# Performance work log

Measured on AMD Instinct MI355X. Metric: run time of the kernel, lower is better.

## Reference

```python
import jax, jax.numpy as jnp
import numpy as np

N_SPECIES = 2
N_RBF = 16
HIDDEN = 64
CUTOFF = 2.5


def setup_inputs() -> dict:
    key = jax.random.key(0)
    ks = jax.random.split(key, 10)
    B, N = 8, 1024
    positions = jax.random.uniform(ks[0], (B, N, 3), dtype=jnp.float32) * 10.0
    types = jax.random.randint(ks[1], (B, N), 0, N_SPECIES)
    in_dim = N_SPECIES + N_SPECIES * N_RBF  # 34
    def lin(k, fan_in, fan_out):
        bound = 1.0 / np.sqrt(fan_in)
        kw, kb = jax.random.split(k)
        W = jax.random.uniform(kw, (fan_in, fan_out), minval=-bound, maxval=bound, dtype=jnp.float32)
        b = jax.random.uniform(kb, (fan_out,), minval=-bound, maxval=bound, dtype=jnp.float32)
        return W, b
    W1, b1 = lin(ks[2], in_dim, 64)
    W2, b2 = lin(ks[3], 64, 64)
    W3, b3 = lin(ks[4], 64, HIDDEN)
    return {"positions": positions, "types": types,
            "W1": W1, "b1": b1, "W2": W2, "b2": b2, "W3": W3, "b3": b3}


def _forward(positions, types, W1, b1, W2, b2, W3, b3):
    B, N, _ = positions.shape
    # pairwise distances with safe sqrt (zero grad on diagonal, matching torch norm subgradient)
    disp = positions[:, :, None, :] - positions[:, None, :, :]          # [B,N,N,3]
    sq = jnp.sum(disp * disp, axis=-1)                                   # [B,N,N]
    nz = sq > 0.0
    d = jnp.sqrt(jnp.where(nz, sq, 1.0)) * nz
    # RBF expansion
    centers = jnp.linspace(0.0, CUTOFF, N_RBF)
    widths = jnp.full((N_RBF,), CUTOFF / max(N_RBF - 1, 1))
    diff = d[..., None] - centers                                        # [B,N,N,R]
    rbf = jnp.exp(-(diff ** 2) / (widths ** 2 + 1e-12))
    # smooth polynomial cutoff
    x = d / CUTOFF
    cut = jnp.where(d < CUTOFF, 1.0 - 6.0 * x ** 5 + 15.0 * x ** 4 - 10.0 * x ** 3, 0.0)
    rbf = rbf * cut[..., None]
    eye = jnp.eye(N, dtype=bool)[None, :, :, None]
    rbf = jnp.where(eye, 0.0, rbf)
    # species-weighted neighbor aggregation
    onehot = jax.nn.one_hot(types, N_SPECIES, dtype=positions.dtype)      # [B,N,S]
    env = jnp.einsum('bijr,bjs->birs', rbf, onehot).reshape(B, N, -1)     # [B,N,R*S]
    feats = jnp.concatenate([onehot, env], axis=-1)                       # [B,N,S+S*R]
    h = jax.nn.silu(feats @ W1 + b1)
    h = jax.nn.silu(h @ W2 + b2)
    return h @ W3 + b3                                                    # [B,N,HIDDEN]


def reference(positions, types, W1, b1, W2, b2, W3, b3):
    return _forward(positions, types, W1, b1, W2, b2, W3, b3)
```

## Files before the change

kernel.cpp:

```cpp
#include <hip/hip_runtime.h>
#include <hip/hip_bf16.h>

#define NTHREADS 256
#define N_ATOMS  1024
#define HIDDEN   64
#define SEGCAP   272

__global__ __launch_bounds__(NTHREADS) void LocalFeatureEncoder_40063454937486_kernel(
    const float* __restrict__ pos,
    const int*   __restrict__ types,
    const float* __restrict__ W1,
    const float* __restrict__ b1,
    const float* __restrict__ W2,
    const float* __restrict__ b2,
    const float* __restrict__ W3,
    const float* __restrict__ b3,
    float*       __restrict__ out)
{
    const int a    = blockIdx.x;
    const int bidx = a >> 10;
    const int i    = a & (N_ATOMS - 1);
    const int tid  = threadIdx.x;
    const int lane = tid & 63;
    const int wav  = tid >> 6;

    __shared__ float2 qdm[4 * SEGCAP];
    __shared__ float2 part2[4 * 16];
    __shared__ int    nseg[4];
    __shared__ float  feats[64];
    __shared__ float  h1s[64];
    __shared__ float  h2s[64];

    const float* pf   = pos + (size_t)bidx * (N_ATOMS * 3);
    const int*   typb = types + (size_t)bidx * N_ATOMS;

    const float4 p0 = *(const float4*)(pf + tid * 12);
    const float4 p1 = *(const float4*)(pf + tid * 12 + 4);
    const float4 p2 = *(const float4*)(pf + tid * 12 + 8);
    const int4   tv = *(const int4*)(typb + tid * 4);

    const float xi = pf[i * 3 + 0];
    const float yi = pf[i * 3 + 1];
    const float zi = pf[i * 3 + 2];

    {
        const float px[4] = {p0.x, p0.w, p1.z, p2.y};
        const float py[4] = {p0.y, p1.x, p1.w, p2.z};
        const float pz[4] = {p0.z, p1.y, p2.x, p2.w};
        const int   tj[4] = {tv.x, tv.y, tv.z, tv.w};
        float2* seg = &qdm[wav * SEGCAP];
        int base = 0;

#pragma unroll
        for (int q = 0; q < 4; ++q) {
            const int j = tid * 4 + q;
            const float dx = xi - px[q], dy = yi - py[q], dz = zi - pz[q];
            const float sq = dx * dx + dy * dy + dz * dz;
            const bool pred = (j != i) && (sq < 6.25f);

            const unsigned long long mask = __ballot(pred);
            if (pred) {
                const float d  = sqrtf(sq);
                const float x  = d * 0.4f;
                const float x3 = x * x * x;
                const float cutv = 1.0f + x3 * (-10.0f + x * (15.0f - 6.0f * x));
                const int idx = base + (int)__popcll(mask & ((1ull << lane) - 1ull));
                seg[idx] = make_float2(d, (tj[q] == 0) ? cutv : -cutv);
            }
            base += (int)__popcll(mask);
        }
        const int npad = (base + 15) & ~15;
        if (lane < npad - base) seg[base + lane] = make_float2(0.0f, 0.0f);
        if (lane == 0) nseg[wav] = npad;
    }
    __syncthreads();

    {
        const int   p = tid >> 4;
        const int   r = tid & 15;
        const float c = (float)r * (2.5f / 15.0f);

        float acc0 = 0.0f, acc1 = 0.0f;
#pragma unroll
        for (int w = 0; w < 4; ++w) {
            const int n = nseg[w];
            const float2* s = &qdm[w * SEGCAP];
            for (int e = p; e < n; e += 16) {
                const float2 dm  = s[e];
                const float diff = dm.x - c;
                const float ex   = __expf(diff * diff * -36.0f);
                acc0 += ex * fmaxf(dm.y, 0.0f);
                acc1 += ex * fmaxf(-dm.y, 0.0f);
            }
        }
        acc0 += __shfl_xor(acc0, 16, 64);
        acc0 += __shfl_xor(acc0, 32, 64);
        acc1 += __shfl_xor(acc1, 16, 64);
        acc1 += __shfl_xor(acc1, 32, 64);
        if (lane < 16) part2[wav * 16 + lane] = make_float2(acc0, acc1);
    }
    __syncthreads();

    if (tid < 16) {
        const float2 a0 = part2[tid];
        const float2 a1 = part2[16 + tid];
        const float2 a2 = part2[32 + tid];
        const float2 a3 = part2[48 + tid];
        feats[2 + 2 * tid + 0] = a0.x + a1.x + a2.x + a3.x;
        feats[2 + 2 * tid + 1] = a0.y + a1.y + a2.y + a3.y;
    }
    if (tid == 16) {
        const int ti = typb[i];
        feats[0] = (ti == 0) ? 1.0f : 0.0f;
        feats[1] = (ti == 1) ? 1.0f : 0.0f;
    }
    __syncthreads();

    if (tid < HIDDEN) {
        float h = b1[tid];
#pragma unroll
        for (int k = 0; k < 34; k++) h += feats[k] * W1[k * HIDDEN + tid];
        h = h / (1.0f + __expf(-h));
        h1s[tid] = h;
    }
    __syncthreads();
    if (tid < HIDDEN) {
        float h = b2[tid];
#pragma unroll
        for (int k = 0; k < HIDDEN; k++) h += h1s[k] * W2[k * HIDDEN + tid];
        h = h / (1.0f + __expf(-h));
        h2s[tid] = h;
    }
    __syncthreads();
    if (tid < HIDDEN) {
        float o = b3[tid];
#pragma unroll
        for (int k = 0; k < HIDDEN; k++) o += h2s[k] * W3[k * HIDDEN + tid];
        out[(size_t)a * HIDDEN + tid] = o;
    }
}

extern "C" void kernel_launch(void* const* d_in, const int* in_sizes, int n_in,
                              void* d_out, int out_size, void* d_ws, size_t ws_size,
                              hipStream_t stream) {
    const float* pos   = (const float*)d_in[0];
    const int*   types = (const int*)d_in[1];
    const float* W1    = (const float*)d_in[2];
    const float* b1    = (const float*)d_in[3];
    const float* W2    = (const float*)d_in[4];
    const float* b2    = (const float*)d_in[5];
    const float* W3    = (const float*)d_in[6];
    const float* b3    = (const float*)d_in[7];
    float*       out   = (float*)d_out;

    const int BN = in_sizes[1];

    LocalFeatureEncoder_40063454937486_kernel<<<BN, NTHREADS, 0, stream>>>(
        pos, types, W1, b1, W2, b2, W3, b3, out);
}
```

Measured before the change: 89.34 us.

## Map one atom per wavefront, stage positions in LDS, use shuffles for MLP

Changes the work split from one atom per 256-thread block to one atom per 64-lane wavefront, with four atoms per block. The block stages all positions and types of its batch in shared memory. Each wave compacts its own neighbour list by scanning all 1024 atoms, evaluates the RBF and cutoff terms from packed signed distances, and runs the three MLP layers with wave shuffles instead of shared-memory barriers. This cuts redundant position loads and MLP-phase idle threads, but each wave now does the full neighbour scan serially and MLP weights are loaded per wave.

```diff
diff --git a/kernel.cpp b/kernel.cpp
--- a/kernel.cpp
+++ b/kernel.cpp
@@ -4,7 +4,7 @@
 #define NTHREADS 256
 #define N_ATOMS  1024
 #define HIDDEN   64
-#define SEGCAP   272
+#define SEGCAP   512
 
 __global__ __launch_bounds__(NTHREADS) void LocalFeatureEncoder_40063454937486_kernel(
     const float* __restrict__ pos,
@@ -17,127 +17,120 @@
     const float* __restrict__ b3,
     float*       __restrict__ out)
 {
-    const int a    = blockIdx.x;
-    const int bidx = a >> 10;
-    const int i    = a & (N_ATOMS - 1);
     const int tid  = threadIdx.x;
     const int lane = tid & 63;
     const int wav  = tid >> 6;
+    const int a    = blockIdx.x * 4 + wav;
+    const int bidx = blockIdx.x >> 8;
+    const int i    = a & (N_ATOMS - 1);
 
-    __shared__ float2 qdm[4 * SEGCAP];
-    __shared__ float2 part2[4 * 16];
-    __shared__ int    nseg[4];
-    __shared__ float  feats[64];
-    __shared__ float  h1s[64];
-    __shared__ float  h2s[64];
+    __shared__ float sx[N_ATOMS];
+    __shared__ float sy[N_ATOMS];
+    __shared__ float sz[N_ATOMS];
+    __shared__ float st[N_ATOMS];
+    __shared__ float qv[4 * SEGCAP];
 
     const float* pf   = pos + (size_t)bidx * (N_ATOMS * 3);
     const int*   typb = types + (size_t)bidx * N_ATOMS;
 
-    const float4 p0 = *(const float4*)(pf + tid * 12);
-    const float4 p1 = *(const float4*)(pf + tid * 12 + 4);
-    const float4 p2 = *(const float4*)(pf + tid * 12 + 8);
-    const int4   tv = *(const int4*)(typb + tid * 4);
+    {
+        const float4 p0 = *(const float4*)(pf + tid * 12);
+        const float4 p1 = *(const float4*)(pf + tid * 12 + 4);
+        const float4 p2 = *(const float4*)(pf + tid * 12 + 8);
+        const int4   tv = *(const int4*)(typb + tid * 4);
 
-    const float xi = pf[i * 3 + 0];
-    const float yi = pf[i * 3 + 1];
-    const float zi = pf[i * 3 + 2];
-
-    {
         const float px[4] = {p0.x, p0.w, p1.z, p2.y};
         const float py[4] = {p0.y, p1.x, p1.w, p2.z};
         const float pz[4] = {p0.z, p1.y, p2.x, p2.w};
         const int   tj[4] = {tv.x, tv.y, tv.z, tv.w};
-        float2* seg = &qdm[wav * SEGCAP];
-        int base = 0;
-
 #pragma unroll
         for (int q = 0; q < 4; ++q) {
             const int j = tid * 4 + q;
-            const float dx = xi - px[q], dy = yi - py[q], dz = zi - pz[q];
-            const float sq = dx * dx + dy * dy + dz * dz;
-            const bool pred = (j != i) && (sq < 6.25f);
-
-            const unsigned long long mask = __ballot(pred);
-            if (pred) {
-                const float d  = sqrtf(sq);
-                const float x  = d * 0.4f;
-                const float x3 = x * x * x;
-                const float cutv = 1.0f + x3 * (-10.0f + x * (15.0f - 6.0f * x));
-                const int idx = base + (int)__popcll(mask & ((1ull << lane) - 1ull));
-                seg[idx] = make_float2(d, (tj[q] == 0) ? cutv : -cutv);
-            }
-            base += (int)__popcll(mask);
+            sx[j] = px[q];
+            sy[j] = py[q];
+            sz[j] = pz[q];
+            st[j] = (tj[q] == 0) ? 1.0f : -1.0f;
         }
-        const int npad = (base + 15) & ~15;
-        if (lane < npad - base) seg[base + lane] = make_float2(0.0f, 0.0f);
-        if (lane == 0) nseg[wav] = npad;
     }
     __syncthreads();
 
-    {
-        const int   p = tid >> 4;
-        const int   r = tid & 15;
-        const float c = (float)r * (2.5f / 15.0f);
+    const float xi = sx[i];
+    const float yi = sy[i];
+    const float zi = sz[i];
 
-        float acc0 = 0.0f, acc1 = 0.0f;
+    float* seg = &qv[wav * SEGCAP];
+    int base = 0;
 #pragma unroll
-        for (int w = 0; w < 4; ++w) {
-            const int n = nseg[w];
-            const float2* s = &qdm[w * SEGCAP];
-            for (int e = p; e < n; e += 16) {
-                const float2 dm  = s[e];
-                const float diff = dm.x - c;
-                const float ex   = __expf(diff * diff * -36.0f);
-                acc0 += ex * fmaxf(dm.y, 0.0f);
-                acc1 += ex * fmaxf(-dm.y, 0.0f);
-            }
+    for (int s = 0; s < N_ATOMS / 64; ++s) {
+        const int j = lane + s * 64;
+        const float dx = xi - sx[j];
+        const float dy = yi - sy[j];
+        const float dz = zi - sz[j];
+        const float sq = dx * dx + dy * dy + dz * dz;
+        const bool pred = (j != i) && (sq < 6.25f);
+
+        const unsigned long long mask = __ballot(pred);
+        if (pred) {
+            const float d = sqrtf(sq);
+            const int idx = base + (int)__popcll(mask & ((1ull << lane) - 1ull));
+            seg[idx] = (st[j] > 0.0f) ? d : -d;
         }
-        acc0 += __shfl_xor(acc0, 16, 64);
-        acc0 += __shfl_xor(acc0, 32, 64);
-        acc1 += __shfl_xor(acc1, 16, 64);
-        acc1 += __shfl_xor(acc1, 32, 64);
-        if (lane < 16) part2[wav * 16 + lane] = make_float2(acc0, acc1);
+        base += (int)__popcll(mask);
     }
+    const int npad = (base + 3) & ~3;
+    if (lane < npad - base) seg[base + lane] = 100.0f;
     __syncthreads();
 
-    if (tid < 16) {
-        const float2 a0 = part2[tid];
-        const float2 a1 = part2[16 + tid];
-        const float2 a2 = part2[32 + tid];
-        const float2 a3 = part2[48 + tid];
-        feats[2 + 2 * tid + 0] = a0.x + a1.x + a2.x + a3.x;
-        feats[2 + 2 * tid + 1] = a0.y + a1.y + a2.y + a3.y;
+    float acc0 = 0.0f, acc1 = 0.0f;
+    {
+        const int   p = lane >> 4;
+        const int   r = lane & 15;
+        const float c = (float)r * (2.5f / 15.0f);
+        const int   slot = p;
+        for (int e = slot; e < npad; e += 4) {
+            const float v   = seg[e];
+            const float d   = fabsf(v);
+            const float sgn = __builtin_copysignf(1.0f, v);
+            const float x   = d * 0.4f;
+            const float x3  = x * x * x;
+            const float cutv = 1.0f + x3 * (-10.0f + x * (15.0f - 6.0f * x));
+            const float diff = d - c;
+            const float ex   = __expf(diff * diff * -36.0f);
+            const float m0 = (sgn > 0.0f) ? cutv : 0.0f;
+            const float m1 = (sgn > 0.0f) ? 0.0f : cutv;
+            acc0 += ex * m0;
+            acc1 += ex * m1;
+        }
     }
-    if (tid == 16) {
-        const int ti = typb[i];
-        feats[0] = (ti == 0) ? 1.0f : 0.0f;
-        feats[1] = (ti == 1) ? 1.0f : 0.0f;
+    acc0 += __shfl_xor(acc0, 16, 64);
+    acc0 += __shfl_xor(acc0, 32, 64);
+    acc1 += __shfl_xor(acc1, 16, 64);
+    acc1 += __shfl_xor(acc1, 32, 64);
+
+    const int t  = lane;
+    const int ti = (st[i] < 0.0f) ? 1 : 0;
+
+    float h1 = b1[t] + W1[ti * HIDDEN + t];
+#pragma unroll
+    for (int r = 0; r < 16; ++r) {
+        h1 += __shfl(acc0, r, 64) * W1[(2 + 2 * r + 0) * HIDDEN + t];
+        h1 += __shfl(acc1, r, 64) * W1[(2 + 2 * r + 1) * HIDDEN + t];
     }
-    __syncthreads();
+    h1 = h1 / (1.0f + __expf(-h1));
 
-    if (tid < HIDDEN) {
-        float h = b1[tid];
+    float h2 = b2[t];
 #pragma unroll
-        for (int k = 0; k < 34; k++) h += feats[k] * W1[k * HIDDEN + tid];
-        h = h / (1.0f + __expf(-h));
-        h1s[tid] = h;
+    for (int k = 0; k < HIDDEN; ++k) {
+        h2 += __shfl(h1, k, 64) * W2[k * HIDDEN + t];
     }
-    __syncthreads();
-    if (tid < HIDDEN) {
-        float h = b2[tid];
+    h2 = h2 / (1.0f + __expf(-h2));
+
+    float o = b3[t];
 #pragma unroll
-        for (int k = 0; k < HIDDEN; k++) h += h1s[k] * W2[k * HIDDEN + tid];
-        h = h / (1.0f + __expf(-h));
-        h2s[tid] = h;
+    for (int k = 0; k < HIDDEN; ++k) {
+        o += __shfl(h2, k, 64) * W3[k * HIDDEN + t];
     }
-    __syncthreads();
-    if (tid < HIDDEN) {
-        float o = b3[tid];
-#pragma unroll
-        for (int k = 0; k < HIDDEN; k++) o += h2s[k] * W3[k * HIDDEN + tid];
-        out[(size_t)a * HIDDEN + tid] = o;
-    }
+    out[(size_t)a * HIDDEN + t] = o;
 }
 
 extern "C" void kernel_launch(void* const* d_in, const int* in_sizes, int n_in,
@@ -155,6 +148,6 @@
 
     const int BN = in_sizes[1];
 
-    LocalFeatureEncoder_40063454937486_kernel<<<BN, NTHREADS, 0, stream>>>(
+    LocalFeatureEncoder_40063454937486_kernel<<<BN / 4, NTHREADS, 0, stream>>>(
         pos, types, W1, b1, W2, b2, W3, b3, out);
 }
```

Result: no change. 89.28 us (-0.1%).
